# Kernel optimization log

Measured on AMD Instinct MI355X. Metric: run time of the kernel, lower is better.

Reference implementation:

```python
import jax, jax.numpy as jnp
import numpy as np

B, H, S, E, MODES = 16, 8, 4096, 64, 64
STD = 0.02 / np.sqrt(E)


def setup_inputs() -> dict:
    key = jax.random.key(0)
    kx, kr, ki, kidx = jax.random.split(key, 4)
    x = jax.random.normal(kx, (B, H, S, E), dtype=jnp.float32)
    weights_real = jax.random.normal(kr, (E, E, MODES), dtype=jnp.float32) * STD
    weights_imag = jax.random.normal(ki, (E, E, MODES), dtype=jnp.float32) * STD
    # torch.randperm(seq_len//2)[:modes].sort(): unique sorted indices in [0, S//2)
    index = jnp.sort(jax.random.permutation(kidx, S // 2)[:MODES]).astype(jnp.int64)
    return {"x": x, "weights_real": weights_real, "weights_imag": weights_imag, "index": index}


def reference(x, weights_real, weights_imag, index):
    seq_len = x.shape[2]
    xt = jnp.swapaxes(x, -1, -2)                      # [B,H,E,S]
    x_ft = jnp.fft.rfft(xt, axis=-1)                  # [B,H,E,S//2+1] complex64
    w = weights_real + 1j * weights_imag              # [E,E,MODES]
    selected = x_ft[..., index]                       # gather -> [B,H,E,MODES]
    processed = jnp.einsum('bhei,eoi->bhoi', selected, w)
    out_ft = jnp.zeros_like(x_ft).at[..., index].set(processed)
    out = jnp.fft.irfft(out_ft, n=seq_len, axis=-1)   # [B,H,E,S]
    return jnp.swapaxes(out, -1, -2)                  # [B,H,S,E]
```

## Files before the change

kernel.cpp:

```cpp
#include <hip/hip_runtime.h>

#define S_LEN 4096
#define E_DIM 64
#define MODES 64
#define BH    128
#define NCH   4
#define CH    1024
#define BK    64

typedef __attribute__((ext_vector_type(8))) short bf16x8;
typedef __attribute__((ext_vector_type(4))) float f32x4;
typedef __attribute__((ext_vector_type(4))) _Float16 f16x4;

__device__ inline unsigned short f2bf(float f) {
    unsigned int u = __float_as_uint(f);
    unsigned int r = u + 0x7FFFu + ((u >> 16) & 1u);
    return (unsigned short)(r >> 16);
}

__device__ inline int posP(int c) { return ((c & 3) << 4) | (c >> 2); }

__global__ __launch_bounds__(256) void k_twp(const int* __restrict__ idx,
                                             const float* __restrict__ wr,
                                             const float* __restrict__ wi,
                                             unsigned short* __restrict__ Tf,
                                             unsigned short* __restrict__ Ui,
                                             unsigned int* __restrict__ Wq) {
    if (blockIdx.x < 1024) {
        int id = blockIdx.x * 256 + threadIdx.x;
        int j = id >> 12;
        int s = id & (S_LEN - 1);
        int m = (idx[j] * s) & (S_LEN - 1);
        float ang = (float)m * (6.283185307179586476925287f / (float)S_LEN);
        float sv, cv;
        __sincosf(ang, &sv, &cv);
        const int tb = (s >> 5) * 4096 + ((s >> 3) & 3) * 128 + (s & 7);
        Tf[tb + ((j >> 4) * 64 + (j & 15)) * 8]              = f2bf(cv);
        Tf[tb + ((4 + (j >> 4)) * 64 + (j & 15)) * 8]        = f2bf(-sv);
        const int ub = (s >> 4) * 2048 + (s & 15) * 8;
        const int qc = ((j >> 3) & 3) * 128 + (j & 7);
        Ui[ub + (j >> 5) * 512 + qc]                          = f2bf(cv);
        Ui[ub + (2 + (j >> 5)) * 512 + qc]                    = f2bf(sv);
    } else {
        const int i = (blockIdx.x - 1024) * 256 + threadIdx.x;
        const int k = i & 63;
        const int o = (i >> 6) & 63;
        const int e = i >> 12;
        const unsigned int pk = (unsigned int)f2bf(wr[i]) | ((unsigned int)f2bf(wi[i]) << 16);
        Wq[(size_t)(o >> 1) * 8192 + e * 128 + k * 2 + (o & 1)] = pk;
    }
}

__global__ __launch_bounds__(512) void k_fwd(const float* __restrict__ x,
                                             const unsigned short* __restrict__ Tf,
                                             _Float16* __restrict__ xfp) {
    __shared__ unsigned short Xs[2][8 * 64 * 8];
    const int bh = blockIdx.x >> 2;
    const int c  = blockIdx.x & 3;
    const int t  = threadIdx.x;
    const int w  = t >> 6;
    const int l  = t & 63;
    const int lr = l & 15;
    const int lg = l >> 4;
    const int q  = l & 15;
    const int h  = l >> 4;
    const int NIT = CH / BK;

    f32x4 acc[4];
    #pragma unroll
    for (int i = 0; i < 4; ++i) { acc[i][0]=0.f; acc[i][1]=0.f; acc[i][2]=0.f; acc[i][3]=0.f; }

    const float* xb = x + ((size_t)bh * S_LEN + c * CH) * E_DIM;
    const unsigned short* Tw = Tf + (size_t)(c * 32) * 4096 + w * 512 + l * 8;
    const float* xg0 = xb + (size_t)(w * 8 + h) * E_DIM + 4 * q;
    const int so = w * 512 + q * 8 + h;

    f32x4 xv[2];
    {
        f32x4 a0 = __builtin_nontemporal_load((const f32x4*)xg0);
        f32x4 a1 = __builtin_nontemporal_load((const f32x4*)(xg0 + 256));
        #pragma unroll
        for (int i = 0; i < 4; ++i) {
            Xs[0][so + i * 128 + 0] = f2bf(a0[i]);
            Xs[0][so + i * 128 + 4] = f2bf(a1[i]);
        }
        xv[0] = __builtin_nontemporal_load((const f32x4*)(xg0 + 4096));
        xv[1] = __builtin_nontemporal_load((const f32x4*)(xg0 + 4096 + 256));
    }
    __syncthreads();

    #pragma unroll 2
    for (int ks = 0; ks < NIT; ++ks) {
        const int p = ks & 1;
        if (ks + 1 < NIT) {
            #pragma unroll
            for (int i = 0; i < 4; ++i) {
                Xs[p ^ 1][so + i * 128 + 0] = f2bf(xv[0][i]);
                Xs[p ^ 1][so + i * 128 + 4] = f2bf(xv[1][i]);
            }
            if (ks + 2 < NIT) {
                const float* xg = xg0 + (size_t)(ks + 2) * 4096;
                xv[0] = __builtin_nontemporal_load((const f32x4*)xg);
                xv[1] = __builtin_nontemporal_load((const f32x4*)(xg + 256));
            }
        }
        #pragma unroll
        for (int ksub = 0; ksub < 2; ++ksub) {
            const bf16x8 af = *(const bf16x8*)&Tw[(size_t)(ks * 2 + ksub) * 4096];
            #pragma unroll
            for (int nt = 0; nt < 4; ++nt) {
                const bf16x8 bfr = *(const bf16x8*)&Xs[p][((ksub * 4 + lg) * 64 + nt * 16 + lr) * 8];
                acc[nt] = __builtin_amdgcn_mfma_f32_16x16x32_bf16(af, bfr, acc[nt], 0, 0, 0);
            }
        }
        __syncthreads();
    }
    _Float16* ob = xfp + ((size_t)c * BH + bh) * 8192;
    #pragma unroll
    for (int r = 0; r < 4; ++r) {
        f16x4 v;
        v[0] = (_Float16)acc[0][r]; v[1] = (_Float16)acc[1][r];
        v[2] = (_Float16)acc[2][r]; v[3] = (_Float16)acc[3][r];
        *(f16x4*)&ob[(size_t)(16 * w + lg * 4 + r) * 64 + 4 * lr] = v;
    }
}

__global__ __launch_bounds__(512) void k_mix(const _Float16* __restrict__ xfp,
                                             const unsigned int* __restrict__ Wq,
                                             const int* __restrict__ idx,
                                             unsigned short* __restrict__ Qpk) {
    __shared__ float xf[2 * 64 * 128];
    const int g   = blockIdx.x;
    const int bhp = g & 63;
    const int ob4 = g >> 6;
    const int t   = threadIdx.x;
    const size_t P = (size_t)BH * 8192;
    #pragma unroll
    for (int b = 0; b < 2; ++b) {
        const _Float16* x0 = xfp + (size_t)(2 * bhp + b) * 8192;
        float* xl = xf + b * 8192;
        #pragma unroll
        for (int i = 0; i < 4; ++i) {
            const int off = i * 2048 + t * 4;
            const int mm  = off >> 6;
            const int e4  = off & 63;
            f16x4 v0 = *(const f16x4*)(x0 + off);
            f16x4 v1 = *(const f16x4*)(x0 + P + off);
            f16x4 v2 = *(const f16x4*)(x0 + 2 * P + off);
            f16x4 v3 = *(const f16x4*)(x0 + 3 * P + off);
            float4 v;
            v.x = ((float)v0[0] + (float)v1[0]) + ((float)v2[0] + (float)v3[0]);
            v.y = ((float)v0[1] + (float)v1[1]) + ((float)v2[1] + (float)v3[1]);
            v.z = ((float)v0[2] + (float)v1[2]) + ((float)v2[2] + (float)v3[2]);
            v.w = ((float)v0[3] + (float)v1[3]) + ((float)v2[3] + (float)v3[3]);
            xl[(e4 + 0) * 128 + (mm ^ (((e4 + 0) >> 2) & 31))] = v.x;
            xl[(e4 + 1) * 128 + (mm ^ (((e4 + 1) >> 2) & 31))] = v.y;
            xl[(e4 + 2) * 128 + (mm ^ (((e4 + 2) >> 2) & 31))] = v.z;
            xl[(e4 + 3) * 128 + (mm ^ (((e4 + 3) >> 2) & 31))] = v.w;
        }
    }
    __syncthreads();
    const int k    = t & 63;
    const int osub = t >> 6;
    const int o0   = ob4 * 16 + osub * 2;
    float pr0[2] = {0.f, 0.f}, pi0[2] = {0.f, 0.f};
    float pr1[2] = {0.f, 0.f}, pi1[2] = {0.f, 0.f};
    const unsigned int* wq = Wq + (size_t)(o0 >> 1) * 8192 + k * 2;
    #pragma unroll 8
    for (int e = 0; e < E_DIM; ++e) {
        const uint2 wv = *(const uint2*)&wq[e * 128];
        const unsigned int w0 = wv.x;
        const unsigned int w1 = wv.y;
        const float a0 = __uint_as_float(w0 << 16);
        const float b0 = __uint_as_float(w0 & 0xFFFF0000u);
        const float a1 = __uint_as_float(w1 << 16);
        const float b1 = __uint_as_float(w1 & 0xFFFF0000u);
        const int swz = (e >> 2) & 31;
        #pragma unroll
        for (int b = 0; b < 2; ++b) {
            const float Xr = xf[b * 8192 + e * 128 + (k ^ swz)];
            const float Xi = xf[b * 8192 + e * 128 + 64 + (k ^ swz)];
            pr0[b] = fmaf(Xr, a0, fmaf(-Xi, b0, pr0[b]));
            pi0[b] = fmaf(Xr, b0, fmaf( Xi, a0, pi0[b]));
            pr1[b] = fmaf(Xr, a1, fmaf(-Xi, b1, pr1[b]));
            pi1[b] = fmaf(Xr, b1, fmaf( Xi, a1, pi1[b]));
        }
    }
    const float sc = (idx[k] == 0 ? 1.0f : 2.0f) / (float)S_LEN;
    const int kp = k >> 3, kl = k & 7;
    const int P0 = posP(o0), P1 = posP(o0 + 1);
    #pragma unroll
    for (int b = 0; b < 2; ++b) {
        unsigned short* qb = Qpk + (size_t)(2 * bhp + b) * 8192;
        qb[(kp * 64 + P0) * 8 + kl]       = f2bf(sc * pr0[b]);
        qb[(kp * 64 + P1) * 8 + kl]       = f2bf(sc * pr1[b]);
        qb[((8 + kp) * 64 + P0) * 8 + kl] = f2bf(-sc * pi0[b]);
        qb[((8 + kp) * 64 + P1) * 8 + kl] = f2bf(-sc * pi1[b]);
    }
}

__global__ __launch_bounds__(256) void k_inv(const unsigned short* __restrict__ Qpk,
                                             const unsigned short* __restrict__ Ui,
                                             float* __restrict__ out) {
    const int g  = blockIdx.x;
    const int bh = (g & 7) | ((g >> 8) << 3);
    const int sc = (g >> 3) & 31;
    const int t  = threadIdx.x;
    const int w  = t >> 6;
    const int l  = t & 63;
    const int lr = l & 15;
    const int lg = l >> 4;

    const unsigned short* qb = Qpk + (size_t)bh * 8192;
    const unsigned short* U0 = Ui + (size_t)(sc * 8 + w * 2) * 2048 + l * 8;

    f32x4 acc[2][4];
    #pragma unroll
    for (int a = 0; a < 2; ++a)
        #pragma unroll
        for (int b = 0; b < 4; ++b) { acc[a][b][0]=0.f; acc[a][b][1]=0.f; acc[a][b][2]=0.f; acc[a][b][3]=0.f; }

    #pragma unroll
    for (int ksb = 0; ksb < 4; ++ksb) {
        const bf16x8 af0 = *(const bf16x8*)&U0[ksb * 512];
        const bf16x8 af1 = *(const bf16x8*)&U0[2048 + ksb * 512];
        #pragma unroll
        for (int nt = 0; nt < 4; ++nt) {
            const bf16x8 bfr = *(const bf16x8*)&qb[((ksb * 4 + lg) * 64 + nt * 16 + lr) * 8];
            acc[0][nt] = __builtin_amdgcn_mfma_f32_16x16x32_bf16(af0, bfr, acc[0][nt], 0, 0, 0);
            acc[1][nt] = __builtin_amdgcn_mfma_f32_16x16x32_bf16(af1, bfr, acc[1][nt], 0, 0, 0);
        }
    }
    float* ob = out + ((size_t)bh * S_LEN + sc * 128) * E_DIM;
    #pragma unroll
    for (int mt = 0; mt < 2; ++mt)
        #pragma unroll
        for (int r = 0; r < 4; ++r) {
            f32x4 v;
            v[0] = acc[mt][0][r]; v[1] = acc[mt][1][r];
            v[2] = acc[mt][2][r]; v[3] = acc[mt][3][r];
            __builtin_nontemporal_store(v,
                (f32x4*)&ob[(size_t)(w * 32 + mt * 16 + lg * 4 + r) * E_DIM + 4 * lr]);
        }
}

extern "C" void kernel_launch(void* const* d_in, const int* in_sizes, int n_in,
                              void* d_out, int out_size, void* d_ws, size_t ws_size,
                              hipStream_t stream) {
    const float* x  = (const float*)d_in[0];
    const float* wr = (const float*)d_in[1];
    const float* wi = (const float*)d_in[2];
    const int*  idx = (const int*)d_in[3];
    float* outp = (float*)d_out;
    char*  ws   = (char*)d_ws;

    unsigned short* Tf  = (unsigned short*)(ws);
    unsigned short* Ui  = (unsigned short*)(ws + (1u << 20));
    _Float16*       xfp = (_Float16*)(ws + (2u << 20));
    unsigned short* Qpk = (unsigned short*)(ws + (10u << 20));
    unsigned int*   Wq  = (unsigned int*)(ws + (12u << 20));

    hipLaunchKernelGGL(k_twp, dim3(2048), dim3(256), 0, stream,
                       idx, wr, wi, Tf, Ui, Wq);
    hipLaunchKernelGGL(k_fwd, dim3(BH * NCH), dim3(512), 0, stream,
                       x, Tf, xfp);
    hipLaunchKernelGGL(k_mix, dim3(256), dim3(512), 0, stream,
                       xfp, Wq, idx, Qpk);
    hipLaunchKernelGGL(k_inv, dim3(BH * 32), dim3(256), 0, stream,
                       Qpk, Ui, outp);
}
```

Before: 69.79 us.

## Move inverse-twiddle and weight packing into forward kernel; widen mix loads

The inverse twiddle table (Ui) and packed weights (Wq) are now produced by extra blocks appended to the forward-DFT kernel, not by the setup kernel. The setup kernel shrinks to building only the forward twiddles that k_fwd needs. That work can then overlap with the forward transform instead of sitting on the critical path before it. Separately, k_mix reads its partial sums with 8-wide half-precision loads instead of 4-wide. The extra blocks in k_fwd carry its shared-memory allocation, which may limit how many can be resident.

```diff
diff --git a/kernel.cpp b/kernel.cpp
--- a/kernel.cpp
+++ b/kernel.cpp
@@ -11,6 +11,7 @@
 typedef __attribute__((ext_vector_type(8))) short bf16x8;
 typedef __attribute__((ext_vector_type(4))) float f32x4;
 typedef __attribute__((ext_vector_type(4))) _Float16 f16x4;
+typedef __attribute__((ext_vector_type(8))) _Float16 f16x8;
 
 __device__ inline unsigned short f2bf(float f) {
     unsigned int u = __float_as_uint(f);
@@ -21,40 +22,51 @@
 __device__ inline int posP(int c) { return ((c & 3) << 4) | (c >> 2); }
 
 __global__ __launch_bounds__(256) void k_twp(const int* __restrict__ idx,
+                                             unsigned short* __restrict__ Tf) {
+    int id = blockIdx.x * 256 + threadIdx.x;
+    int j = id >> 12;
+    int s = id & (S_LEN - 1);
+    int m = (idx[j] * s) & (S_LEN - 1);
+    float ang = (float)m * (6.283185307179586476925287f / (float)S_LEN);
+    float sv, cv;
+    __sincosf(ang, &sv, &cv);
+    const int tb = (s >> 5) * 4096 + ((s >> 3) & 3) * 128 + (s & 7);
+    Tf[tb + ((j >> 4) * 64 + (j & 15)) * 8]       = f2bf(cv);
+    Tf[tb + ((4 + (j >> 4)) * 64 + (j & 15)) * 8] = f2bf(-sv);
+}
+
+__global__ __launch_bounds__(512) void k_fwd(const float* __restrict__ x,
+                                             const unsigned short* __restrict__ Tf,
+                                             _Float16* __restrict__ xfp,
+                                             const int* __restrict__ idx,
                                              const float* __restrict__ wr,
                                              const float* __restrict__ wi,
-                                             unsigned short* __restrict__ Tf,
                                              unsigned short* __restrict__ Ui,
                                              unsigned int* __restrict__ Wq) {
-    if (blockIdx.x < 1024) {
-        int id = blockIdx.x * 256 + threadIdx.x;
-        int j = id >> 12;
-        int s = id & (S_LEN - 1);
-        int m = (idx[j] * s) & (S_LEN - 1);
-        float ang = (float)m * (6.283185307179586476925287f / (float)S_LEN);
-        float sv, cv;
-        __sincosf(ang, &sv, &cv);
-        const int tb = (s >> 5) * 4096 + ((s >> 3) & 3) * 128 + (s & 7);
-        Tf[tb + ((j >> 4) * 64 + (j & 15)) * 8]              = f2bf(cv);
-        Tf[tb + ((4 + (j >> 4)) * 64 + (j & 15)) * 8]        = f2bf(-sv);
-        const int ub = (s >> 4) * 2048 + (s & 15) * 8;
-        const int qc = ((j >> 3) & 3) * 128 + (j & 7);
-        Ui[ub + (j >> 5) * 512 + qc]                          = f2bf(cv);
-        Ui[ub + (2 + (j >> 5)) * 512 + qc]                    = f2bf(sv);
-    } else {
-        const int i = (blockIdx.x - 1024) * 256 + threadIdx.x;
+    __shared__ unsigned short Xs[2][8 * 64 * 8];
+    if (blockIdx.x >= 1024) {
+        const int i = (blockIdx.x - 1024) * 512 + threadIdx.x;
         const int k = i & 63;
         const int o = (i >> 6) & 63;
         const int e = i >> 12;
         const unsigned int pk = (unsigned int)f2bf(wr[i]) | ((unsigned int)f2bf(wi[i]) << 16);
         Wq[(size_t)(o >> 1) * 8192 + e * 128 + k * 2 + (o & 1)] = pk;
-    }
-}
-
-__global__ __launch_bounds__(512) void k_fwd(const float* __restrict__ x,
-                                             const unsigned short* __restrict__ Tf,
-                                             _Float16* __restrict__ xfp) {
-    __shared__ unsigned short Xs[2][8 * 64 * 8];
+        return;
+    }
+    if (blockIdx.x >= 512) {
+        const int id = (blockIdx.x - 512) * 512 + threadIdx.x;
+        const int j = id >> 12;
+        const int s = id & (S_LEN - 1);
+        const int m = (idx[j] * s) & (S_LEN - 1);
+        float ang = (float)m * (6.283185307179586476925287f / (float)S_LEN);
+        float sv, cv;
+        __sincosf(ang, &sv, &cv);
+        const int ub = (s >> 4) * 2048 + (s & 15) * 8;
+        const int qc = ((j >> 3) & 3) * 128 + (j & 7);
+        Ui[ub + (j >> 5) * 512 + qc]       = f2bf(cv);
+        Ui[ub + (2 + (j >> 5)) * 512 + qc] = f2bf(sv);
+        return;
+    }
     const int bh = blockIdx.x >> 2;
     const int c  = blockIdx.x & 3;
     const int t  = threadIdx.x;
@@ -140,23 +152,20 @@
         const _Float16* x0 = xfp + (size_t)(2 * bhp + b) * 8192;
         float* xl = xf + b * 8192;
         #pragma unroll
-        for (int i = 0; i < 4; ++i) {
-            const int off = i * 2048 + t * 4;
+        for (int i = 0; i < 2; ++i) {
+            const int off = i * 4096 + t * 8;
             const int mm  = off >> 6;
             const int e4  = off & 63;
-            f16x4 v0 = *(const f16x4*)(x0 + off);
-            f16x4 v1 = *(const f16x4*)(x0 + P + off);
-            f16x4 v2 = *(const f16x4*)(x0 + 2 * P + off);
-            f16x4 v3 = *(const f16x4*)(x0 + 3 * P + off);
-            float4 v;
-            v.x = ((float)v0[0] + (float)v1[0]) + ((float)v2[0] + (float)v3[0]);
-            v.y = ((float)v0[1] + (float)v1[1]) + ((float)v2[1] + (float)v3[1]);
-            v.z = ((float)v0[2] + (float)v1[2]) + ((float)v2[2] + (float)v3[2]);
-            v.w = ((float)v0[3] + (float)v1[3]) + ((float)v2[3] + (float)v3[3]);
-            xl[(e4 + 0) * 128 + (mm ^ (((e4 + 0) >> 2) & 31))] = v.x;
-            xl[(e4 + 1) * 128 + (mm ^ (((e4 + 1) >> 2) & 31))] = v.y;
-            xl[(e4 + 2) * 128 + (mm ^ (((e4 + 2) >> 2) & 31))] = v.z;
-            xl[(e4 + 3) * 128 + (mm ^ (((e4 + 3) >> 2) & 31))] = v.w;
+            f16x8 v0 = *(const f16x8*)(x0 + off);
+            f16x8 v1 = *(const f16x8*)(x0 + P + off);
+            f16x8 v2 = *(const f16x8*)(x0 + 2 * P + off);
+            f16x8 v3 = *(const f16x8*)(x0 + 3 * P + off);
+            #pragma unroll
+            for (int j = 0; j < 8; ++j) {
+                const float sv = ((float)v0[j] + (float)v1[j]) + ((float)v2[j] + (float)v3[j]);
+                const int e = e4 + j;
+                xl[e * 128 + (mm ^ ((e >> 2) & 31))] = sv;
+            }
         }
     }
     __syncthreads();
@@ -260,10 +269,10 @@
     unsigned short* Qpk = (unsigned short*)(ws + (10u << 20));
     unsigned int*   Wq  = (unsigned int*)(ws + (12u << 20));
 
-    hipLaunchKernelGGL(k_twp, dim3(2048), dim3(256), 0, stream,
-                       idx, wr, wi, Tf, Ui, Wq);
-    hipLaunchKernelGGL(k_fwd, dim3(BH * NCH), dim3(512), 0, stream,
-                       x, Tf, xfp);
+    hipLaunchKernelGGL(k_twp, dim3(1024), dim3(256), 0, stream,
+                       idx, Tf);
+    hipLaunchKernelGGL(k_fwd, dim3(512 + 1024), dim3(512), 0, stream,
+                       x, Tf, xfp, idx, wr, wi, Ui, Wq);
     hipLaunchKernelGGL(k_mix, dim3(256), dim3(512), 0, stream,
                        xfp, Wq, idx, Qpk);
     hipLaunchKernelGGL(k_inv, dim3(BH * 32), dim3(256), 0, stream,
```

Measured after the change: 72.14 us. +3.4%, slower.
